# Optimization experiments

Measured on AMD Instinct MI355X. Metric: run time of the kernel, lower is better.

Reference implementation:

```python
import jax, jax.numpy as jnp
import numpy as np

GROUP_SIZE = 128   # GPTQ quantization group size
LORA_SCALING = 32.0 / 16.0  # lora_alpha / r


def setup_inputs() -> dict:
    key = jax.random.key(0)
    k1, k2, k3, k4, k5, k6 = jax.random.split(key, 6)
    B, S, D_in, D_out, R = 4, 2048, 4096, 4096, 16
    n_groups = D_in // GROUP_SIZE
    x = jax.random.normal(k1, (B, S, D_in), dtype=jnp.float32)
    qweight = jax.random.randint(k2, (D_in, D_out), 0, 16, dtype=jnp.int32)
    qzeros = jax.random.randint(k3, (n_groups, D_out), 0, 16, dtype=jnp.int32)
    scales = jax.random.uniform(k4, (n_groups, D_out), dtype=jnp.float32) * 0.01
    lora_A = jax.random.normal(k5, (R, D_in), dtype=jnp.float32) * 0.02
    lora_B = jax.random.normal(k6, (D_out, R), dtype=jnp.float32) * 0.02
    return {"x": x, "qweight": qweight, "qzeros": qzeros,
            "scales": scales, "lora_A": lora_A, "lora_B": lora_B}


def reference(x, qweight, qzeros, scales, lora_A, lora_B):
    # --- GPTQ dequantize: W[i,o] = (q[i,o] - zero[g(i),o]) * scale[g(i),o] ---
    scale_full = jnp.repeat(scales, GROUP_SIZE, axis=0)              # [D_in, D_out]
    zero_full = jnp.repeat(qzeros, GROUP_SIZE, axis=0)               # [D_in, D_out]
    W = (qweight - zero_full).astype(x.dtype) * scale_full           # [D_in, D_out]
    # --- base quantized linear ---
    result = jnp.einsum('bsi,io->bso', x, W)                         # [B, S, D_out]
    # --- LoRA branch (dropout p=0 -> identity): B(A(x)) * scaling ---
    ax = jnp.einsum('bsi,ri->bsr', x, lora_A)                        # [B, S, R]
    lora_out = jnp.einsum('bsr,or->bso', ax, lora_B) * LORA_SCALING  # [B, S, D_out]
    return (result + lora_out).astype(result.dtype)
```

## Files before the change

kernel.cpp:

```cpp
#include <hip/hip_runtime.h>
#include <stdint.h>


#define GM 8192
#define GN 4096
#define GK 4096
#define RLORA 16
#define LSCALE 2.0f
#define NSLAB 128

typedef __attribute__((ext_vector_type(4))) float f32x4;
typedef __attribute__((ext_vector_type(8))) _Float16 half8;
typedef __attribute__((ext_vector_type(8))) uint16_t u16x8;
typedef __attribute__((ext_vector_type(4))) uint16_t u16x4;

#define BAR() asm volatile("s_barrier" ::: "memory")
#define VMCNT8() do { asm volatile("s_waitcnt vmcnt(8)" ::: "memory"); \
                      __builtin_amdgcn_sched_barrier(0); } while (0)
#define VMCNT0() do { asm volatile("s_waitcnt vmcnt(0)" ::: "memory"); \
                      __builtin_amdgcn_sched_barrier(0); } while (0)

__device__ __forceinline__ uint16_t f2h(float f) {
  union { _Float16 h; uint16_t u; } c;
  c.h = (_Float16)f;
  return c.u;
}

__device__ __forceinline__ void async16(const void* g, void* l) {
  __builtin_amdgcn_global_load_lds(
      (const __attribute__((address_space(1))) void*)g,
      (__attribute__((address_space(3))) void*)l, 16, 0, 0);
}

__global__ void prep_w_k(const int* __restrict__ qw, const int* __restrict__ qz,
                         const float* __restrict__ sc, const float* __restrict__ lA,
                         uint16_t* __restrict__ wt, uint16_t* __restrict__ laq) {
  int tid = threadIdx.x;
  if (blockIdx.x >= (GK / 64) * (GN / 64)) {
    int b = blockIdx.x - (GK / 64) * (GN / 64);
#pragma unroll
    for (int i = 0; i < 32; ++i) {
      int c = b * 8192 + i * 256 + tid;
      f32x4 v = ((const f32x4*)lA)[c];
      u16x4 h;
#pragma unroll
      for (int q = 0; q < 4; ++q) h[q] = f2h(v[q]);
      ((u16x4*)laq)[c] = h;
    }
    return;
  }
  __shared__ uint16_t t[64][66];
  int bn = blockIdx.x % (GN / 64);
  int bk = blockIdx.x / (GN / 64);
  int k0 = bk * 64, n0 = bn * 64;
  int g = k0 >> 7;
  int n = tid & 63;
  int kb = tid >> 6;
  int z = qz[g * GN + n0 + n];
  float s = sc[g * GN + n0 + n];
#pragma unroll
  for (int i = 0; i < 16; ++i) {
    int kk = kb + i * 4;
    int q = qw[(size_t)(k0 + kk) * GN + n0 + n];
    t[kk][n] = f2h((float)(q - z) * s);
  }
  __syncthreads();
  for (int c = tid; c < 512; c += 256) {
    int nn = c >> 3;
    int k8 = (c & 7) * 8;
    u16x8 v;
#pragma unroll
    for (int j = 0; j < 8; ++j) v[j] = t[k8 + j][nn];
    *(u16x8*)&wt[(size_t)(n0 + nn) * GK + k0 + k8] = v;
  }
}

__global__ __launch_bounds__(256) void prep_xax_k(
    const float* __restrict__ x, const uint16_t* __restrict__ laq,
    uint16_t* __restrict__ xq, float* __restrict__ axw) {
  __shared__ float red[4][16][17];
  int tid = threadIdx.x;
  int w = tid >> 6, lane = tid & 63;
  int m0 = blockIdx.x * 16;
  int kq = w * 1024;
#pragma unroll
  for (int i = 0; i < 16; ++i) {
#pragma unroll
    for (int j = 0; j < 4; ++j) {
      size_t off = (size_t)(m0 + i) * GK + kq + j * 256 + lane * 4;
      f32x4 v = *(const f32x4*)&x[off];
      u16x4 h;
#pragma unroll
      for (int q = 0; q < 4; ++q) h[q] = f2h(v[q]);
      *(u16x4*)&xq[off] = h;
    }
  }
  VMCNT0();
  int fr = lane & 15, fk = lane >> 4;
  f32x4 acc = {0.f, 0.f, 0.f, 0.f};
  const uint16_t* xrow = xq + (size_t)(m0 + fr) * GK + kq + fk * 8;
  const uint16_t* arow = laq + (size_t)fr * GK + kq + fk * 8;
#pragma unroll 4
  for (int s = 0; s < 32; ++s) {
    half8 av = *(const half8*)(xrow + s * 32);
    half8 bv = *(const half8*)(arow + s * 32);
    acc = __builtin_amdgcn_mfma_f32_16x16x32_f16(av, bv, acc, 0, 0, 0);
  }
#pragma unroll
  for (int e = 0; e < 4; ++e) red[w][fk * 4 + e][fr] = acc[e];
  __syncthreads();
  int row = tid >> 4, col = tid & 15;
  if (tid < 256) {
    float sum = red[0][row][col] + red[1][row][col] +
                red[2][row][col] + red[3][row][col];
    axw[(size_t)(m0 + row) * RLORA + col] = sum;
  }
}

__global__ __launch_bounds__(512, 2) void gemm_k(
    const uint16_t* __restrict__ xq, const uint16_t* __restrict__ wt,
    const float* __restrict__ axw, const float* __restrict__ lB,
    float* __restrict__ out) {
  __shared__ __align__(16) uint16_t sA[4 * 8192];
  __shared__ __align__(16) uint16_t sB[4 * 8192];

  const int nbx = GN / 256;
  int wg = blockIdx.x;
  int swz = (wg & 7) * 64 + (wg >> 3);
  int by = swz / nbx, bx = swz % nbx;
  int m0 = by * 256, n0 = bx * 256;

  int tid = threadIdx.x;
  int w = tid >> 6, lane = tid & 63;
  int wm = w >> 2, wn = w & 3;
  int fr = lane & 15, fk = lane >> 4;

  size_t aSrc[2], bSrc[2];
  int dstOff[2];
#pragma unroll
  for (int j = 0; j < 2; ++j) {
    int c = (j * 8 + w) * 64 + lane;
    int row = c >> 2;
    int kl = (c & 3) ^ ((row >> 1) & 3);
    aSrc[j] = (size_t)(m0 + row) * GK + kl * 8;
    bSrc[j] = (size_t)(n0 + row) * GK + kl * 8;
    dstOff[j] = (j * 8 + w) * 512;
  }

  int aOff[8], bOff[4];
#pragma unroll
  for (int mi = 0; mi < 8; ++mi) {
    int r = wm * 128 + mi * 16 + fr;
    aOff[mi] = r * 32 + ((fk ^ ((r >> 1) & 3)) << 3);
  }
#pragma unroll
  for (int ni = 0; ni < 4; ++ni) {
    int r = wn * 64 + ni * 16 + fr;
    bOff[ni] = r * 32 + ((fk ^ ((r >> 1) & 3)) << 3);
  }

#pragma unroll
  for (int t = 0; t < 3; ++t) {
    async16(xq + aSrc[0] + t * 32, sA + t * 8192 + dstOff[0]);
    async16(xq + aSrc[1] + t * 32, sA + t * 8192 + dstOff[1]);
    async16(wt + bSrc[0] + t * 32, sB + t * 8192 + dstOff[0]);
    async16(wt + bSrc[1] + t * 32, sB + t * 8192 + dstOff[1]);
  }

  f32x4 acc[8][4];
#pragma unroll
  for (int a = 0; a < 8; ++a)
#pragma unroll
    for (int b = 0; b < 4; ++b)
#pragma unroll
      for (int e = 0; e < 4; ++e) acc[a][b][e] = 0.f;

  VMCNT8();
  BAR();

#pragma unroll 4
  for (int g = 0; g < NSLAB; ++g) {
    const uint16_t* sa = sA + (g & 3) * 8192;
    const uint16_t* sb = sB + (g & 3) * 8192;
    int t2 = g + 3;
    int tc = (t2 < NSLAB ? t2 : NSLAB - 1) * 32;
    uint16_t* dA = sA + (t2 & 3) * 8192;
    uint16_t* dB = sB + (t2 & 3) * 8192;

    half8 b0[4], a0[4];
#pragma unroll
    for (int ni = 0; ni < 4; ++ni) b0[ni] = *(const half8*)(sb + bOff[ni]);
#pragma unroll
    for (int mi = 0; mi < 4; ++mi) a0[mi] = *(const half8*)(sa + aOff[mi]);
    async16(xq + aSrc[0] + tc, dA + dstOff[0]);
    async16(xq + aSrc[1] + tc, dA + dstOff[1]);
    __builtin_amdgcn_s_setprio(1);
#pragma unroll
    for (int mi = 0; mi < 4; ++mi)
#pragma unroll
      for (int ni = 0; ni < 4; ++ni)
        acc[mi][ni] = __builtin_amdgcn_mfma_f32_16x16x32_f16(
            a0[mi], b0[ni], acc[mi][ni], 0, 0, 0);
    __builtin_amdgcn_s_setprio(0);

    half8 a1[4];
#pragma unroll
    for (int mi = 0; mi < 4; ++mi) a1[mi] = *(const half8*)(sa + aOff[4 + mi]);
    async16(wt + bSrc[0] + tc, dB + dstOff[0]);
    async16(wt + bSrc[1] + tc, dB + dstOff[1]);
    VMCNT8();
    __builtin_amdgcn_s_setprio(1);
#pragma unroll
    for (int mi = 0; mi < 4; ++mi)
#pragma unroll
      for (int ni = 0; ni < 4; ++ni)
        acc[4 + mi][ni] = __builtin_amdgcn_mfma_f32_16x16x32_f16(
            a1[mi], b0[ni], acc[4 + mi][ni], 0, 0, 0);
    __builtin_amdgcn_s_setprio(0);
    BAR();
  }

  VMCNT0();
  __syncthreads();
  float* sax = (float*)sA;
  float* slb = (float*)sB;
  for (int c = tid; c < 1024; c += 512) {
    int row = c >> 2, q = c & 3;
    ((f32x4*)sax)[c] = *(const f32x4*)&axw[(size_t)(m0 + row) * RLORA + q * 4];
    ((f32x4*)slb)[c] = *(const f32x4*)&lB[(size_t)(n0 + row) * RLORA + q * 4];
  }
  __syncthreads();
  f32x4 lbv[4][4];
#pragma unroll
  for (int ni = 0; ni < 4; ++ni) {
    int nl = wn * 64 + ni * 16 + fr;
#pragma unroll
    for (int q = 0; q < 4; ++q) lbv[ni][q] = ((const f32x4*)&slb[nl * 16])[q];
  }
#pragma unroll
  for (int mi = 0; mi < 8; ++mi) {
#pragma unroll
    for (int e = 0; e < 4; ++e) {
      int mr = wm * 128 + mi * 16 + fk * 4 + e;
      f32x4 axq[4];
#pragma unroll
      for (int q = 0; q < 4; ++q) axq[q] = ((const f32x4*)&sax[mr * 16])[q];
      float* orow = out + (size_t)(m0 + mr) * GN + n0 + wn * 64;
#pragma unroll
      for (int ni = 0; ni < 4; ++ni) {
        float d = 0.f;
#pragma unroll
        for (int q = 0; q < 4; ++q) {
          f32x4 p = axq[q] * lbv[ni][q];
          d += p[0] + p[1] + p[2] + p[3];
        }
        orow[ni * 16 + fr] = acc[mi][ni][e] + LSCALE * d;
      }
    }
  }
}

__global__ void fb_gemm_k(const float* __restrict__ x, const int* __restrict__ qw,
                          const int* __restrict__ qz, const float* __restrict__ sc,
                          float* __restrict__ out) {
  __shared__ float sx[32][33];
  int nbx = GN / 32;
  int bx = blockIdx.x % nbx, by = blockIdx.x / nbx;
  int tid = threadIdx.x;
  int tn = tid & 31, tg = tid >> 5;
  float acc[4] = {0.f, 0.f, 0.f, 0.f};
  int n = bx * 32 + tn;
  for (int k0 = 0; k0 < GK; k0 += 32) {
    for (int i = tid; i < 32 * 32; i += 256)
      sx[i >> 5][i & 31] = x[(size_t)(by * 32 + (i >> 5)) * GK + k0 + (i & 31)];
    __syncthreads();
    int g = k0 >> 7;
    float z = (float)qz[g * GN + n];
    float s = sc[g * GN + n];
    for (int kk = 0; kk < 32; ++kk) {
      float wv = ((float)qw[(size_t)(k0 + kk) * GN + n] - z) * s;
#pragma unroll
      for (int mm = 0; mm < 4; ++mm) acc[mm] += sx[tg * 4 + mm][kk] * wv;
    }
    __syncthreads();
  }
#pragma unroll
  for (int mm = 0; mm < 4; ++mm)
    out[(size_t)(by * 32 + tg * 4 + mm) * GN + n] = acc[mm];
}

__global__ void fb_lora_k(const float* __restrict__ x, const float* __restrict__ lA,
                          const float* __restrict__ lB, float* __restrict__ out) {
  int m = blockIdx.x;
  int tid = threadIdx.x;
  __shared__ float red[256];
  __shared__ float sax[RLORA];
  for (int r = 0; r < RLORA; ++r) {
    float a = 0.f;
    for (int k = tid; k < GK; k += 256)
      a += x[(size_t)m * GK + k] * lA[(size_t)r * GK + k];
    red[tid] = a;
    __syncthreads();
    for (int off2 = 128; off2 > 0; off2 >>= 1) {
      if (tid < off2) red[tid] += red[tid + off2];
      __syncthreads();
    }
    if (tid == 0) sax[r] = red[0];
    __syncthreads();
  }
  for (int nn = tid; nn < GN; nn += 256) {
    float d = 0.f;
#pragma unroll
    for (int r = 0; r < RLORA; ++r) d += sax[r] * lB[(size_t)nn * RLORA + r];
    out[(size_t)m * GN + nn] += LSCALE * d;
  }
}

extern "C" void kernel_launch(void* const* d_in, const int* in_sizes, int n_in,
                              void* d_out, int out_size, void* d_ws, size_t ws_size,
                              hipStream_t stream) {
  const float* x = (const float*)d_in[0];
  const int* qw = (const int*)d_in[1];
  const int* qz = (const int*)d_in[2];
  const float* sc = (const float*)d_in[3];
  const float* lA = (const float*)d_in[4];
  const float* lB = (const float*)d_in[5];
  float* out = (float*)d_out;

  const size_t XQ = 0;
  const size_t WT = (size_t)GM * GK * 2;
  const size_t AX = WT + (size_t)GN * GK * 2;
  const size_t LQ = AX + (size_t)GM * RLORA * 4;
  const size_t TOT = LQ + (size_t)RLORA * GK * 2;

  if (ws_size >= TOT) {
    uint16_t* xq = (uint16_t*)((char*)d_ws + XQ);
    uint16_t* wt = (uint16_t*)((char*)d_ws + WT);
    float* ax = (float*)((char*)d_ws + AX);
    uint16_t* laq = (uint16_t*)((char*)d_ws + LQ);
    hipLaunchKernelGGL(prep_w_k, dim3((GK / 64) * (GN / 64) + 2), dim3(256), 0,
                       stream, qw, qz, sc, lA, wt, laq);
    hipLaunchKernelGGL(prep_xax_k, dim3(GM / 16), dim3(256), 0, stream,
                       x, laq, xq, ax);
    hipLaunchKernelGGL(gemm_k, dim3((GM / 256) * (GN / 256)), dim3(512), 0, stream,
                       xq, wt, ax, lB, out);
  } else {
    hipLaunchKernelGGL(fb_gemm_k, dim3((GM / 32) * (GN / 32)), dim3(256), 0, stream,
                       x, qw, qz, sc, out);
    hipLaunchKernelGGL(fb_lora_k, dim3(GM), dim3(256), 0, stream, x, lA, lB, out);
  }
}
```

Before: 546.2 us.

## Switch main GEMM to 32x32x16 MFMA and stage LoRA-A matmul through LDS

The main GEMM now uses 32x32x16 f16 MFMA tiles in place of 16x16x32, with the LDS swizzle, fragment offsets, accumulator layout and epilogue row mapping rewritten to match. Larger MFMA tiles need fewer LDS fragment reads per FLOP and fewer MFMA issues. Separately, the x-prep kernel now converts x to fp16 into LDS and async-loads lora_A chunks into swizzled LDS, instead of re-reading the fp16 x and lora_A from global memory. It also gains an occupancy hint of 2 blocks per SM. The swizzle changes carry a risk of new LDS bank conflicts.

```diff
diff --git a/kernel.cpp b/kernel.cpp
--- a/kernel.cpp
+++ b/kernel.cpp
@@ -10,6 +10,7 @@
 #define NSLAB 128
 
 typedef __attribute__((ext_vector_type(4))) float f32x4;
+typedef __attribute__((ext_vector_type(16))) float f32x16;
 typedef __attribute__((ext_vector_type(8))) _Float16 half8;
 typedef __attribute__((ext_vector_type(8))) uint16_t u16x8;
 typedef __attribute__((ext_vector_type(4))) uint16_t u16x4;
@@ -19,6 +20,8 @@
                       __builtin_amdgcn_sched_barrier(0); } while (0)
 #define VMCNT0() do { asm volatile("s_waitcnt vmcnt(0)" ::: "memory"); \
                       __builtin_amdgcn_sched_barrier(0); } while (0)
+#define WAITALL() do { asm volatile("s_waitcnt vmcnt(0) lgkmcnt(0)" ::: "memory"); \
+                       __builtin_amdgcn_sched_barrier(0); } while (0)
 
 __device__ __forceinline__ uint16_t f2h(float f) {
   union { _Float16 h; uint16_t u; } c;
@@ -75,46 +78,57 @@
   }
 }
 
-__global__ __launch_bounds__(256) void prep_xax_k(
+__global__ __launch_bounds__(256, 2) void prep_xax_k(
     const float* __restrict__ x, const uint16_t* __restrict__ laq,
     uint16_t* __restrict__ xq, float* __restrict__ axw) {
+  __shared__ __align__(16) uint16_t At[4][16 * 264];
+  __shared__ __align__(16) uint16_t Bt[4][16 * 256];
   __shared__ float red[4][16][17];
   int tid = threadIdx.x;
   int w = tid >> 6, lane = tid & 63;
   int m0 = blockIdx.x * 16;
   int kq = w * 1024;
-#pragma unroll
-  for (int i = 0; i < 16; ++i) {
-#pragma unroll
-    for (int j = 0; j < 4; ++j) {
-      size_t off = (size_t)(m0 + i) * GK + kq + j * 256 + lane * 4;
+  int fr = lane & 15, fk = lane >> 4;
+  uint16_t* at = At[w];
+  uint16_t* bt = Bt[w];
+  f32x4 acc = {0.f, 0.f, 0.f, 0.f};
+
+  int br = (lane >> 5);
+  for (int c = 0; c < 4; ++c) {
+    int kbase = kq + c * 256;
+#pragma unroll
+    for (int u = 0; u < 8; ++u) {
+      int pos = u * 64 + lane;
+      int r = pos >> 5, p = pos & 31;
+      async16(laq + (size_t)r * GK + kbase + ((p ^ (r & 7)) << 3),
+              bt + u * 512);
+    }
+#pragma unroll 4
+    for (int i = 0; i < 16; ++i) {
+      size_t off = (size_t)(m0 + i) * GK + kbase + lane * 4;
       f32x4 v = *(const f32x4*)&x[off];
       u16x4 h;
 #pragma unroll
       for (int q = 0; q < 4; ++q) h[q] = f2h(v[q]);
       *(u16x4*)&xq[off] = h;
-    }
-  }
-  VMCNT0();
-  int fr = lane & 15, fk = lane >> 4;
-  f32x4 acc = {0.f, 0.f, 0.f, 0.f};
-  const uint16_t* xrow = xq + (size_t)(m0 + fr) * GK + kq + fk * 8;
-  const uint16_t* arow = laq + (size_t)fr * GK + kq + fk * 8;
-#pragma unroll 4
-  for (int s = 0; s < 32; ++s) {
-    half8 av = *(const half8*)(xrow + s * 32);
-    half8 bv = *(const half8*)(arow + s * 32);
-    acc = __builtin_amdgcn_mfma_f32_16x16x32_f16(av, bv, acc, 0, 0, 0);
-  }
+      *(u16x4*)&at[i * 264 + lane * 4] = h;
+    }
+    WAITALL();
+#pragma unroll
+    for (int s = 0; s < 8; ++s) {
+      half8 av = *(const half8*)&at[fr * 264 + s * 32 + fk * 8];
+      half8 bv = *(const half8*)&bt[fr * 256 + (((s * 4 + fk) ^ (fr & 7)) << 3)];
+      acc = __builtin_amdgcn_mfma_f32_16x16x32_f16(av, bv, acc, 0, 0, 0);
+    }
+  }
+  (void)br;
 #pragma unroll
   for (int e = 0; e < 4; ++e) red[w][fk * 4 + e][fr] = acc[e];
   __syncthreads();
   int row = tid >> 4, col = tid & 15;
-  if (tid < 256) {
-    float sum = red[0][row][col] + red[1][row][col] +
-                red[2][row][col] + red[3][row][col];
-    axw[(size_t)(m0 + row) * RLORA + col] = sum;
-  }
+  float sum = red[0][row][col] + red[1][row][col] +
+              red[2][row][col] + red[3][row][col];
+  axw[(size_t)(m0 + row) * RLORA + col] = sum;
 }
 
 __global__ __launch_bounds__(512, 2) void gemm_k(
@@ -133,7 +147,7 @@
   int tid = threadIdx.x;
   int w = tid >> 6, lane = tid & 63;
   int wm = w >> 2, wn = w & 3;
-  int fr = lane & 15, fk = lane >> 4;
+  int fc = lane & 31, l5 = lane >> 5;
 
   size_t aSrc[2], bSrc[2];
   int dstOff[2];
@@ -141,23 +155,29 @@
   for (int j = 0; j < 2; ++j) {
     int c = (j * 8 + w) * 64 + lane;
     int row = c >> 2;
-    int kl = (c & 3) ^ ((row >> 1) & 3);
+    int kl = (c & 3) ^ ((row >> 2) & 3);
     aSrc[j] = (size_t)(m0 + row) * GK + kl * 8;
     bSrc[j] = (size_t)(n0 + row) * GK + kl * 8;
     dstOff[j] = (j * 8 + w) * 512;
   }
 
-  int aOff[8], bOff[4];
-#pragma unroll
-  for (int mi = 0; mi < 8; ++mi) {
-    int r = wm * 128 + mi * 16 + fr;
-    aOff[mi] = r * 32 + ((fk ^ ((r >> 1) & 3)) << 3);
-  }
-#pragma unroll
-  for (int ni = 0; ni < 4; ++ni) {
-    int r = wn * 64 + ni * 16 + fr;
-    bOff[ni] = r * 32 + ((fk ^ ((r >> 1) & 3)) << 3);
-  }
+  int aOff[4][2], bOff[2][2];
+#pragma unroll
+  for (int mi = 0; mi < 4; ++mi)
+#pragma unroll
+    for (int ks = 0; ks < 2; ++ks) {
+      int r = wm * 128 + mi * 32 + fc;
+      int l = ks * 2 + l5;
+      aOff[mi][ks] = r * 32 + (((l ^ ((r >> 2) & 3))) << 3);
+    }
+#pragma unroll
+  for (int ni = 0; ni < 2; ++ni)
+#pragma unroll
+    for (int ks = 0; ks < 2; ++ks) {
+      int r = wn * 64 + ni * 32 + fc;
+      int l = ks * 2 + l5;
+      bOff[ni][ks] = r * 32 + (((l ^ ((r >> 2) & 3))) << 3);
+    }
 
 #pragma unroll
   for (int t = 0; t < 3; ++t) {
@@ -167,18 +187,18 @@
     async16(wt + bSrc[1] + t * 32, sB + t * 8192 + dstOff[1]);
   }
 
-  f32x4 acc[8][4];
-#pragma unroll
-  for (int a = 0; a < 8; ++a)
-#pragma unroll
-    for (int b = 0; b < 4; ++b)
-#pragma unroll
-      for (int e = 0; e < 4; ++e) acc[a][b][e] = 0.f;
+  f32x16 acc[4][2];
+#pragma unroll
+  for (int a = 0; a < 4; ++a)
+#pragma unroll
+    for (int b = 0; b < 2; ++b)
+#pragma unroll
+      for (int e = 0; e < 16; ++e) acc[a][b][e] = 0.f;
 
   VMCNT8();
   BAR();
 
-#pragma unroll 4
+#pragma unroll 2
   for (int g = 0; g < NSLAB; ++g) {
     const uint16_t* sa = sA + (g & 3) * 8192;
     const uint16_t* sb = sB + (g & 3) * 8192;
@@ -187,25 +207,27 @@
     uint16_t* dA = sA + (t2 & 3) * 8192;
     uint16_t* dB = sB + (t2 & 3) * 8192;
 
-    half8 b0[4], a0[4];
-#pragma unroll
-    for (int ni = 0; ni < 4; ++ni) b0[ni] = *(const half8*)(sb + bOff[ni]);
-#pragma unroll
-    for (int mi = 0; mi < 4; ++mi) a0[mi] = *(const half8*)(sa + aOff[mi]);
+    half8 a0[4], b0[2];
+#pragma unroll
+    for (int ni = 0; ni < 2; ++ni) b0[ni] = *(const half8*)(sb + bOff[ni][0]);
+#pragma unroll
+    for (int mi = 0; mi < 4; ++mi) a0[mi] = *(const half8*)(sa + aOff[mi][0]);
     async16(xq + aSrc[0] + tc, dA + dstOff[0]);
     async16(xq + aSrc[1] + tc, dA + dstOff[1]);
     __builtin_amdgcn_s_setprio(1);
 #pragma unroll
     for (int mi = 0; mi < 4; ++mi)
 #pragma unroll
-      for (int ni = 0; ni < 4; ++ni)
-        acc[mi][ni] = __builtin_amdgcn_mfma_f32_16x16x32_f16(
+      for (int ni = 0; ni < 2; ++ni)
+        acc[mi][ni] = __builtin_amdgcn_mfma_f32_32x32x16_f16(
             a0[mi], b0[ni], acc[mi][ni], 0, 0, 0);
     __builtin_amdgcn_s_setprio(0);
 
-    half8 a1[4];
-#pragma unroll
-    for (int mi = 0; mi < 4; ++mi) a1[mi] = *(const half8*)(sa + aOff[4 + mi]);
+    half8 a1[4], b1[2];
+#pragma unroll
+    for (int ni = 0; ni < 2; ++ni) b1[ni] = *(const half8*)(sb + bOff[ni][1]);
+#pragma unroll
+    for (int mi = 0; mi < 4; ++mi) a1[mi] = *(const half8*)(sa + aOff[mi][1]);
     async16(wt + bSrc[0] + tc, dB + dstOff[0]);
     async16(wt + bSrc[1] + tc, dB + dstOff[1]);
     VMCNT8();
@@ -213,9 +235,9 @@
 #pragma unroll
     for (int mi = 0; mi < 4; ++mi)
 #pragma unroll
-      for (int ni = 0; ni < 4; ++ni)
-        acc[4 + mi][ni] = __builtin_amdgcn_mfma_f32_16x16x32_f16(
-            a1[mi], b0[ni], acc[4 + mi][ni], 0, 0, 0);
+      for (int ni = 0; ni < 2; ++ni)
+        acc[mi][ni] = __builtin_amdgcn_mfma_f32_32x32x16_f16(
+            a1[mi], b1[ni], acc[mi][ni], 0, 0, 0);
     __builtin_amdgcn_s_setprio(0);
     BAR();
   }
@@ -230,31 +252,31 @@
     ((f32x4*)slb)[c] = *(const f32x4*)&lB[(size_t)(n0 + row) * RLORA + q * 4];
   }
   __syncthreads();
-  f32x4 lbv[4][4];
-#pragma unroll
-  for (int ni = 0; ni < 4; ++ni) {
-    int nl = wn * 64 + ni * 16 + fr;
+  f32x4 lbv[2][4];
+#pragma unroll
+  for (int ni = 0; ni < 2; ++ni) {
+    int nl = wn * 64 + ni * 32 + fc;
 #pragma unroll
     for (int q = 0; q < 4; ++q) lbv[ni][q] = ((const f32x4*)&slb[nl * 16])[q];
   }
 #pragma unroll
-  for (int mi = 0; mi < 8; ++mi) {
-#pragma unroll
-    for (int e = 0; e < 4; ++e) {
-      int mr = wm * 128 + mi * 16 + fk * 4 + e;
+  for (int mi = 0; mi < 4; ++mi) {
+#pragma unroll
+    for (int e = 0; e < 16; ++e) {
+      int mr = wm * 128 + mi * 32 + (e & 3) + ((e >> 2) << 3) + (l5 << 2);
       f32x4 axq[4];
 #pragma unroll
       for (int q = 0; q < 4; ++q) axq[q] = ((const f32x4*)&sax[mr * 16])[q];
       float* orow = out + (size_t)(m0 + mr) * GN + n0 + wn * 64;
 #pragma unroll
-      for (int ni = 0; ni < 4; ++ni) {
+      for (int ni = 0; ni < 2; ++ni) {
         float d = 0.f;
 #pragma unroll
         for (int q = 0; q < 4; ++q) {
           f32x4 p = axq[q] * lbv[ni][q];
           d += p[0] + p[1] + p[2] + p[3];
         }
-        orow[ni * 16 + fr] = acc[mi][ni][e] + LSCALE * d;
+        orow[ni * 32 + fc] = acc[mi][ni][e] + LSCALE * d;
       }
     }
   }
```

New measurement: 562.4 us. 1.03x slower.
